# Performance work log

Measured on AMD Instinct MI355X. Metric: run time of the kernel, lower is better.

The kernel has to match this reference:

```python
import jax, jax.numpy as jnp
import numpy as np

B, N, H, W = 8, 500000, 512, 512
HALF_CENTOR = True
BIG = jnp.float32(3.4e38)  # sentinel for invalid points in segment_min


def setup_inputs() -> dict:
    key = jax.random.key(0)
    k1, k2 = jax.random.split(key)
    # continuous (x, y) coords in grid units; slightly out of bounds to exercise the mask
    points = jax.random.uniform(k1, (B, N, 2), minval=-8.0, maxval=520.0, dtype=jnp.float32)
    costs = jax.random.normal(k2, (B, N), dtype=jnp.float32)
    default_cost = jnp.zeros([], jnp.float32)  # trainable scalar (default_type='DYNAMIC')
    return {"points": points, "costs": costs, "default_cost": default_cost,
            "height": H, "width": W}


def reference(points, costs, default_cost, height, width):
    b, n, _ = points.shape
    half = 0.5 if HALF_CENTOR else 0.0
    ix = jnp.floor(points[..., 0] + half).astype(jnp.int32)  # [B, N]
    iy = jnp.floor(points[..., 1] + half).astype(jnp.int32)
    valid = (ix >= 0) & (ix < width) & (iy >= 0) & (iy < height)
    bidx = jnp.broadcast_to(jnp.arange(b, dtype=jnp.int32)[:, None], (b, n))
    nseg = b * height * width
    # invalid points routed to an extra trash segment that is sliced off
    seg = jnp.where(valid, (bidx * height + iy) * width + ix, nseg).reshape(-1)
    cmin = jax.ops.segment_min(jnp.where(valid, costs, BIG).reshape(-1), seg,
                               num_segments=nseg + 1)[:nseg]
    count = jax.ops.segment_sum(valid.reshape(-1).astype(jnp.int32), seg,
                                num_segments=nseg + 1)[:nseg]
    cost_mask = (count - 1).reshape(b, height, width)  # -1 where cell empty (MIN semantics)
    cost = jnp.where(cost_mask >= 0, cmin.reshape(b, height, width), default_cost)
    return cost, cost_mask
```

## Files before the change

kernel.cpp:

```cpp
#include <hip/hip_runtime.h>


#define CHUNK 8192
#define TPB 512
constexpr int HH = 512, WW = 512;
constexpr int NBINS = 512;
constexpr int CAP = 16384;

__device__ __forceinline__ unsigned f2ord(float f) {
    unsigned u = __float_as_uint(f);
    return (u & 0x80000000u) ? ~u : (u | 0x80000000u);
}
__device__ __forceinline__ float ord2f(unsigned u) {
    return __uint_as_float((u & 0x80000000u) ? (u & 0x7FFFFFFFu) : ~u);
}

__global__ void pInit(unsigned* __restrict__ gcur) {
    gcur[threadIdx.x] = (unsigned)(threadIdx.x * CAP);
}

__global__ __launch_bounds__(TPB) void pS(const float2* __restrict__ pts,
                                          const float* __restrict__ costs,
                                          unsigned* __restrict__ gcur,
                                          unsigned* __restrict__ sorted,
                                          int npts, int N) {
    __shared__ unsigned skey[CHUNK];
    __shared__ unsigned hist[NBINS];
    __shared__ unsigned gbase[NBINS];
    __shared__ unsigned lcur[NBINS];
    const int t = threadIdx.x, blk = blockIdx.x;
    hist[t] = 0u;
    lcur[t] = 0u;
    __syncthreads();

    const int base = blk * CHUNK;
    const int b0 = base / N;
    const int boundary = (b0 + 1) * N;

#pragma unroll
    for (int k = 0; k < CHUNK / TPB; ++k) {
        int idx = base + k * TPB + t;
        unsigned key = 0xFFFFFFFFu;
        if (idx < npts) {
            float2 p = pts[idx];
            int ix = (int)floorf(p.x + 0.5f);
            int iy = (int)floorf(p.y + 0.5f);
            if (ix >= 0 && ix < WW && iy >= 0 && iy < HH) {
                int b = (idx >= boundary) ? b0 + 1 : b0;
                unsigned bin = (unsigned)(b * 64 + ((iy >> 6) << 3) + (ix >> 6));
                key = (bin << 12) | (unsigned)(((iy & 63) << 6) | (ix & 63));
                atomicAdd(&hist[bin], 1u);
            }
        }
        skey[k * TPB + t] = key;
    }
    __syncthreads();

    gbase[t] = atomicAdd(&gcur[t], hist[t]);
    __syncthreads();

#pragma unroll
    for (int k = 0; k < CHUNK / TPB; ++k) {
        int idx = base + k * TPB + t;
        if (idx < npts) {
            unsigned key = skey[k * TPB + t];
            if (key != 0xFFFFFFFFu) {
                unsigned bin = key >> 12, lc = key & 4095u;
                unsigned off = atomicAdd(&lcur[bin], 1u);
                unsigned slot = gbase[bin] + off;
                if (slot < (bin + 1u) * CAP)
                    sorted[slot] = (lc << 20) | (f2ord(costs[idx]) >> 12);
            }
        }
    }
}

__global__ __launch_bounds__(TPB) void pD(const unsigned* __restrict__ sorted,
                                          const unsigned* __restrict__ gcur,
                                          const float* __restrict__ def,
                                          float* __restrict__ out_cost,
                                          float* __restrict__ out_mask) {
    __shared__ unsigned mn[4096];
    __shared__ unsigned ct[4096];
    const int bin = blockIdx.x, t = threadIdx.x;
#pragma unroll
    for (int i = t; i < 4096; i += TPB) { mn[i] = 0xFFFFFFFFu; ct[i] = 0u; }
    __syncthreads();
    const unsigned s0 = (unsigned)bin * CAP;
    const unsigned e  = gcur[bin];
    const unsigned s1 = (e < s0 + CAP) ? e : s0 + CAP;
    for (unsigned i = s0 + t; i < s1; i += TPB) {
        unsigned v = sorted[i];
        atomicMin(&mn[v >> 20], v & 0xFFFFFu);
        atomicAdd(&ct[v >> 20], 1u);
    }
    __syncthreads();
    const float d = *def;
    const int b = bin >> 6, tile = bin & 63, ty = tile >> 3, tx = tile & 7;
    const int r = t >> 3, c0 = (t & 7) * 8;
    const int o0 = (b * HH + ty * 64 + r) * WW + tx * 64 + c0;
#pragma unroll
    for (int v4 = 0; v4 < 2; ++v4) {
        float4 oc, om;
        float* pc = (float*)&oc;
        float* pm = (float*)&om;
#pragma unroll
        for (int j = 0; j < 4; ++j) {
            int i = r * 64 + c0 + v4 * 4 + j;
            unsigned c = ct[i];
            pc[j] = c ? ord2f((mn[i] << 12) | 0x800u) : d;
            pm[j] = (float)((int)c - 1);
        }
        *(float4*)(out_cost + o0 + v4 * 4) = oc;
        *(float4*)(out_mask + o0 + v4 * 4) = om;
    }
}

__global__ void fb_init(uint2* __restrict__ cells, int nseg) {
    int i = blockIdx.x * blockDim.x + threadIdx.x;
    int stride = gridDim.x * blockDim.x;
    for (; i < nseg; i += stride) cells[i] = make_uint2(0xFFFFFFFFu, 0u);
}
__global__ void fb_scatter(const float2* __restrict__ pts, const float* __restrict__ costs,
                           uint2* __restrict__ cells, int npts, int N, int H, int W) {
    int i = blockIdx.x * blockDim.x + threadIdx.x;
    if (i >= npts) return;
    float2 p = pts[i];
    int ix = (int)floorf(p.x + 0.5f), iy = (int)floorf(p.y + 0.5f);
    if (ix < 0 || ix >= W || iy < 0 || iy >= H) return;
    int b = i / N;
    atomicMin(&cells[(b * H + iy) * W + ix].x, f2ord(costs[i]));
    atomicAdd(&cells[(b * H + iy) * W + ix].y, 1u);
}
__global__ void fb_final(const uint2* __restrict__ cells, const float* __restrict__ def,
                         float* __restrict__ oc, float* __restrict__ om, int nseg) {
    int i = blockIdx.x * blockDim.x + threadIdx.x;
    if (i >= nseg) return;
    uint2 c = cells[i];
    float d = *def;
    oc[i] = c.y ? ord2f(c.x) : d;
    om[i] = (float)((int)c.y - 1);
}

extern "C" void kernel_launch(void* const* d_in, const int* in_sizes, int n_in,
                              void* d_out, int out_size, void* d_ws, size_t ws_size,
                              hipStream_t stream) {
    const float2* pts = (const float2*)d_in[0];
    const float*  cst = (const float*)d_in[1];
    const float*  def = (const float*)d_in[2];

    const int npts = in_sizes[1];
    const int nseg = out_size / 2;
    const int B    = nseg / (HH * WW);
    const int N    = npts / B;
    float* out_cost = (float*)d_out;
    float* out_mask = out_cost + nseg;

    const int NB = (npts + CHUNK - 1) / CHUNK;
    const size_t sorted_bytes = (size_t)NBINS * CAP * 4;
    const size_t need = sorted_bytes + NBINS * 4;
    const bool cap_ok = (npts / NBINS) * 2 <= CAP;

    if (B == 8 && nseg == 8 * HH * WW && ws_size >= need && N > CHUNK && cap_ok) {
        unsigned* sorted = (unsigned*)d_ws;
        unsigned* gcur   = (unsigned*)((char*)d_ws + sorted_bytes);

        pInit<<<1,     TPB, 0, stream>>>(gcur);
        pS   <<<NB,    TPB, 0, stream>>>(pts, cst, gcur, sorted, npts, N);
        pD   <<<NBINS, TPB, 0, stream>>>(sorted, gcur, def, out_cost, out_mask);
    } else {
        uint2* cells = (uint2*)d_ws;
        fb_init   <<<2048, 256, 0, stream>>>(cells, nseg);
        fb_scatter<<<(npts + 255) / 256, 256, 0, stream>>>(pts, cst, cells, npts, N, HH, WW);
        fb_final  <<<(nseg + 255) / 256, 256, 0, stream>>>(cells, def, out_cost, out_mask, nseg);
    }
}
```

Measured before the change: 123.4 us.

## Keep points in registers and reuse histogram atomic rank in binning kernel

The partition kernel now loads all of a thread's points and costs into registers up front and takes each point's rank from the return value of the histogram atomicAdd. This drops the shared key array, the second local-cursor atomic pass and the second global read of costs. The chunk size is halved so the per-thread register arrays stay small, which doubles the block count and the number of global cursor atomics. Register pressure rises, and the order of writes within a bin changes, which has no effect on min or count.

```diff
diff --git a/kernel.cpp b/kernel.cpp
--- a/kernel.cpp
+++ b/kernel.cpp
@@ -1,8 +1,9 @@
 #include <hip/hip_runtime.h>
 
 
-#define CHUNK 8192
+#define CHUNK 4096
 #define TPB 512
+#define KPT (CHUNK / TPB)
 constexpr int HH = 512, WW = 512;
 constexpr int NBINS = 512;
 constexpr int CAP = 16384;
@@ -24,35 +25,39 @@
                                           unsigned* __restrict__ gcur,
                                           unsigned* __restrict__ sorted,
                                           int npts, int N) {
-    __shared__ unsigned skey[CHUNK];
     __shared__ unsigned hist[NBINS];
     __shared__ unsigned gbase[NBINS];
-    __shared__ unsigned lcur[NBINS];
     const int t = threadIdx.x, blk = blockIdx.x;
     hist[t] = 0u;
-    lcur[t] = 0u;
     __syncthreads();
 
     const int base = blk * CHUNK;
     const int b0 = base / N;
     const int boundary = (b0 + 1) * N;
 
+    float2 p[KPT];
+    float  c[KPT];
 #pragma unroll
-    for (int k = 0; k < CHUNK / TPB; ++k) {
+    for (int k = 0; k < KPT; ++k) {
         int idx = base + k * TPB + t;
-        unsigned key = 0xFFFFFFFFu;
-        if (idx < npts) {
-            float2 p = pts[idx];
-            int ix = (int)floorf(p.x + 0.5f);
-            int iy = (int)floorf(p.y + 0.5f);
-            if (ix >= 0 && ix < WW && iy >= 0 && iy < HH) {
-                int b = (idx >= boundary) ? b0 + 1 : b0;
-                unsigned bin = (unsigned)(b * 64 + ((iy >> 6) << 3) + (ix >> 6));
-                key = (bin << 12) | (unsigned)(((iy & 63) << 6) | (ix & 63));
-                atomicAdd(&hist[bin], 1u);
-            }
+        bool in = idx < npts;
+        p[k] = in ? pts[idx]   : make_float2(-100.f, -100.f);
+        c[k] = in ? costs[idx] : 0.f;
+    }
+    unsigned key[KPT], rank[KPT];
+#pragma unroll
+    for (int k = 0; k < KPT; ++k) {
+        int idx = base + k * TPB + t;
+        int ix = (int)floorf(p[k].x + 0.5f);
+        int iy = (int)floorf(p[k].y + 0.5f);
+        key[k] = 0xFFFFFFFFu;
+        rank[k] = 0u;
+        if (ix >= 0 && ix < WW && iy >= 0 && iy < HH) {
+            int b = (idx >= boundary) ? b0 + 1 : b0;
+            unsigned bin = (unsigned)(b * 64 + ((iy >> 6) << 3) + (ix >> 6));
+            key[k] = (bin << 12) | (unsigned)(((iy & 63) << 6) | (ix & 63));
+            rank[k] = atomicAdd(&hist[bin], 1u);
         }
-        skey[k * TPB + t] = key;
     }
     __syncthreads();
 
@@ -60,17 +65,12 @@
     __syncthreads();
 
 #pragma unroll
-    for (int k = 0; k < CHUNK / TPB; ++k) {
-        int idx = base + k * TPB + t;
-        if (idx < npts) {
-            unsigned key = skey[k * TPB + t];
-            if (key != 0xFFFFFFFFu) {
-                unsigned bin = key >> 12, lc = key & 4095u;
-                unsigned off = atomicAdd(&lcur[bin], 1u);
-                unsigned slot = gbase[bin] + off;
-                if (slot < (bin + 1u) * CAP)
-                    sorted[slot] = (lc << 20) | (f2ord(costs[idx]) >> 12);
-            }
+    for (int k = 0; k < KPT; ++k) {
+        if (key[k] != 0xFFFFFFFFu) {
+            unsigned bin = key[k] >> 12, lc = key[k] & 4095u;
+            unsigned slot = gbase[bin] + rank[k];
+            if (slot < (bin + 1u) * CAP)
+                sorted[slot] = (lc << 20) | (f2ord(c[k]) >> 12);
         }
     }
 }
@@ -107,9 +107,9 @@
 #pragma unroll
         for (int j = 0; j < 4; ++j) {
             int i = r * 64 + c0 + v4 * 4 + j;
-            unsigned c = ct[i];
-            pc[j] = c ? ord2f((mn[i] << 12) | 0x800u) : d;
-            pm[j] = (float)((int)c - 1);
+            unsigned cc = ct[i];
+            pc[j] = cc ? ord2f((mn[i] << 12) | 0x800u) : d;
+            pm[j] = (float)((int)cc - 1);
         }
         *(float4*)(out_cost + o0 + v4 * 4) = oc;
         *(float4*)(out_mask + o0 + v4 * 4) = om;
```

Measured after the change: 129.1 us. 1.05x slower.
